# Optimization experiments

Hardware: AMD Instinct MI355X
Metric: run time of the kernel (lower is better)

## Reference

```python
import jax, jax.numpy as jnp
import numpy as np

LN_EPS = 1e-5


def setup_inputs() -> dict:
    key = jax.random.key(0)
    ks = jax.random.split(key, 8)
    B, N, E = 4, 512, 64
    s = 1.0 / np.sqrt(E)
    node_emb = jax.random.normal(ks[0], (B, N, E), dtype=jnp.float32)
    node_mask = jnp.ones((B, N), dtype=jnp.bool_)  # unused by forward, kept for fidelity
    ln_g = jnp.ones((E,), dtype=jnp.float32)
    ln_b = jnp.zeros((E,), dtype=jnp.float32)
    W1 = jax.random.normal(ks[1], (E, E), dtype=jnp.float32) * s
    b1 = jnp.zeros((E,), dtype=jnp.float32)
    W2 = jax.random.normal(ks[2], (E, E), dtype=jnp.float32) * s
    b2 = jnp.zeros((E,), dtype=jnp.float32)
    Wc = jax.random.normal(ks[3], (E, E * E), dtype=jnp.float32) / np.sqrt(E * E)
    bc = jnp.zeros((E,), dtype=jnp.float32)
    return {"node_emb": node_emb, "node_mask": node_mask, "ln_g": ln_g, "ln_b": ln_b,
            "W1": W1, "b1": b1, "W2": W2, "b2": b2, "Wc": Wc, "bc": bc}


def reference(node_emb, node_mask, ln_g, ln_b, W1, b1, W2, b2, Wc, bc):
    # node_emb: [B, N, E]; node_mask is unused (matches original module).
    E = node_emb.shape[-1]
    # LayerNorm over last dim (biased variance, like torch)
    mu = jnp.mean(node_emb, axis=-1, keepdims=True)
    var = jnp.mean(jnp.square(node_emb - mu), axis=-1, keepdims=True)
    h = (node_emb - mu) * jax.lax.rsqrt(var + LN_EPS) * ln_g + ln_b
    # Gated projections
    x = h * (jnp.einsum('bnd,od->bno', h, W1) + b1)   # left activations  [B,N,E]
    y = h * (jnp.einsum('bnd,od->bno', h, W2) + b2)   # right activations [B,N,E]
    # Original: matmul of [B,N*E,1] @ [B,1,N*E] then reshape/permute; analytically
    # R[b,i,d1,d2,j] = x[b,i,d1] * y[b,j,d2], flattened (d1,d2) fed to lin_cat.
    y2 = jnp.swapaxes(y, 1, 2)                        # [B, E, N]
    Wr = Wc.reshape(E, E, E)                          # Wr[o, d1, d2] = Wc[o, d1*E+d2]
    # Fused lin_cat: out[b,i,j,o] = sum_{d1,d2} x[b,i,d1] * y2[b,d2,j] * Wr[o,d1,d2] + bc[o]
    tmp = jnp.einsum('bid,ode->bioe', x, Wr)          # [B, N, E, E] (small)
    out = jnp.einsum('bioe,bej->bijo', tmp, y2) + bc  # [B, N, N, E]
    return out
```

## Files before the change

### kernel.cpp

```cpp
#include <hip/hip_runtime.h>
#include <hip/hip_bf16.h>


typedef __bf16 bf16x8 __attribute__((ext_vector_type(8)));
typedef unsigned short u16x8 __attribute__((ext_vector_type(8)));
typedef float f32x16 __attribute__((ext_vector_type(16)));

static __device__ inline unsigned short f2bf(float f) {
    unsigned int u = __float_as_uint(f);
    u = (u + 0x7FFFu + ((u >> 16) & 1u)) >> 16;
    return (unsigned short)u;
}

static __device__ inline bf16x8 load_frag(const unsigned short* p) {
    u16x8 t = *(const u16x8*)p;
    return __builtin_bit_cast(bf16x8, t);
}

__global__ __launch_bounds__(256) void ln_gate_kernel(
    const float* __restrict__ emb, const float* __restrict__ g,
    const float* __restrict__ bln,
    const float* __restrict__ W1, const float* __restrict__ b1,
    const float* __restrict__ W2, const float* __restrict__ b2,
    unsigned short* __restrict__ xo, unsigned short* __restrict__ yo)
{
    __shared__ float hsh[4][64];
    const int wave = threadIdx.x >> 6;
    const int lane = threadIdx.x & 63;
    const int row  = blockIdx.x * 4 + wave;

    float e = emb[row * 64 + lane];
    float s = e;
    #pragma unroll
    for (int m = 1; m < 64; m <<= 1) s += __shfl_xor(s, m);
    const float mu = s * (1.0f / 64.0f);
    const float d  = e - mu;
    float v = d * d;
    #pragma unroll
    for (int m = 1; m < 64; m <<= 1) v += __shfl_xor(v, m);
    const float rs = rsqrtf(v * (1.0f / 64.0f) + 1e-5f);
    const float h  = d * rs * g[lane] + bln[lane];

    hsh[wave][lane] = h;
    __syncthreads();

    const float4* hv  = (const float4*)hsh[wave];
    const float4* w1v = (const float4*)(W1 + lane * 64);
    const float4* w2v = (const float4*)(W2 + lane * 64);
    float d1 = 0.f, d2 = 0.f;
    #pragma unroll
    for (int k = 0; k < 16; k++) {
        float4 hh = hv[k];
        float4 a  = w1v[k];
        float4 c  = w2v[k];
        d1 += hh.x * a.x + hh.y * a.y + hh.z * a.z + hh.w * a.w;
        d2 += hh.x * c.x + hh.y * c.y + hh.z * c.z + hh.w * c.w;
    }
    xo[row * 64 + lane] = f2bf(h * (d1 + b1[lane]));
    yo[row * 64 + lane] = f2bf(h * (d2 + b2[lane]));
}

__global__ __launch_bounds__(256) void wcprep_kernel(
    const float* __restrict__ Wc, unsigned short* __restrict__ wt)
{
    __shared__ float t[64][65];
    const int o = blockIdx.x;
    const float* src = Wc + o * 4096;
    for (int w = threadIdx.x; w < 4096; w += 256)
        t[w >> 6][w & 63] = src[w];
    __syncthreads();
    unsigned short* dst = wt + o * 4096;
    for (int w = threadIdx.x; w < 4096; w += 256) {
        int d2 = w >> 6, d1 = w & 63;
        dst[w] = f2bf(t[d1][d2]);
    }
}

__global__ __launch_bounds__(256) void ugemm_kernel(
    const unsigned short* __restrict__ x, const unsigned short* __restrict__ wt,
    unsigned short* __restrict__ u)
{
    const int wave = threadIdx.x >> 6;
    const int lane = threadIdx.x & 63;
    const int m0 = blockIdx.x * 128 + (wave >> 1) * 64;
    const int n0 = blockIdx.y * 128 + (wave & 1) * 64;
    const int lr = lane & 31, lh = lane >> 5;

    bf16x8 af[2][4], bf[2][4];
    #pragma unroll
    for (int ks = 0; ks < 4; ks++) {
        const int k = ks * 16 + lh * 8;
        af[0][ks] = load_frag(x  + (m0      + lr) * 64 + k);
        af[1][ks] = load_frag(x  + (m0 + 32 + lr) * 64 + k);
        bf[0][ks] = load_frag(wt + (n0      + lr) * 64 + k);
        bf[1][ks] = load_frag(wt + (n0 + 32 + lr) * 64 + k);
    }
    f32x16 acc[2][2] = {};
    #pragma unroll
    for (int ks = 0; ks < 4; ks++) {
        acc[0][0] = __builtin_amdgcn_mfma_f32_32x32x16_bf16(af[0][ks], bf[0][ks], acc[0][0], 0, 0, 0);
        acc[0][1] = __builtin_amdgcn_mfma_f32_32x32x16_bf16(af[0][ks], bf[1][ks], acc[0][1], 0, 0, 0);
        acc[1][0] = __builtin_amdgcn_mfma_f32_32x32x16_bf16(af[1][ks], bf[0][ks], acc[1][0], 0, 0, 0);
        acc[1][1] = __builtin_amdgcn_mfma_f32_32x32x16_bf16(af[1][ks], bf[1][ks], acc[1][1], 0, 0, 0);
    }
    #pragma unroll
    for (int mi = 0; mi < 2; mi++)
        #pragma unroll
        for (int ni = 0; ni < 2; ni++)
            #pragma unroll
            for (int r = 0; r < 16; r++) {
                int row = m0 + mi * 32 + (r & 3) + 8 * (r >> 2) + 4 * lh;
                int col = n0 + ni * 32 + lr;
                u[row * 4096 + col] = f2bf(acc[mi][ni][r]);
            }
}

__global__ __launch_bounds__(256) void out_kernel(
    const unsigned short* __restrict__ y, const unsigned short* __restrict__ u,
    const float* __restrict__ bc, float* __restrict__ out)
{
    const int wave = threadIdx.x >> 6;
    const int lane = threadIdx.x & 63;
    const int mp = blockIdx.x;
    const int b  = mp >> 9;
    const int j0 = blockIdx.y * 256 + wave * 64;
    const int lr = lane & 31, lh = lane >> 5;

    const unsigned short* yb = y + b * (512 * 64);
    const unsigned short* ub = u + mp * 4096;

    bf16x8 af[2][4], bf[2][4];
    #pragma unroll
    for (int ks = 0; ks < 4; ks++) {
        const int k = ks * 16 + lh * 8;
        af[0][ks] = load_frag(yb + (j0      + lr) * 64 + k);
        af[1][ks] = load_frag(yb + (j0 + 32 + lr) * 64 + k);
        bf[0][ks] = load_frag(ub + (lr)      * 64 + k);
        bf[1][ks] = load_frag(ub + (32 + lr) * 64 + k);
    }
    f32x16 acc[2][2] = {};
    #pragma unroll
    for (int ks = 0; ks < 4; ks++) {
        acc[0][0] = __builtin_amdgcn_mfma_f32_32x32x16_bf16(af[0][ks], bf[0][ks], acc[0][0], 0, 0, 0);
        acc[0][1] = __builtin_amdgcn_mfma_f32_32x32x16_bf16(af[0][ks], bf[1][ks], acc[0][1], 0, 0, 0);
        acc[1][0] = __builtin_amdgcn_mfma_f32_32x32x16_bf16(af[1][ks], bf[0][ks], acc[1][0], 0, 0, 0);
        acc[1][1] = __builtin_amdgcn_mfma_f32_32x32x16_bf16(af[1][ks], bf[1][ks], acc[1][1], 0, 0, 0);
    }

    const float bias0 = bc[lr];
    const float bias1 = bc[32 + lr];
    float* outp = out + (size_t)mp * 32768;
    #pragma unroll
    for (int mi = 0; mi < 2; mi++)
        #pragma unroll
        for (int ni = 0; ni < 2; ni++) {
            const float bias = ni ? bias1 : bias0;
            const int col = ni * 32 + lr;
            #pragma unroll
            for (int r = 0; r < 16; r++) {
                int j = j0 + mi * 32 + (r & 3) + 8 * (r >> 2) + 4 * lh;
                __builtin_nontemporal_store(acc[mi][ni][r] + bias, &outp[j * 64 + col]);
            }
        }
}

extern "C" void kernel_launch(void* const* d_in, const int* in_sizes, int n_in,
                              void* d_out, int out_size, void* d_ws, size_t ws_size,
                              hipStream_t stream) {
    const float* emb  = (const float*)d_in[0];
    const float* ln_g = (const float*)d_in[2];
    const float* ln_b = (const float*)d_in[3];
    const float* W1   = (const float*)d_in[4];
    const float* b1   = (const float*)d_in[5];
    const float* W2   = (const float*)d_in[6];
    const float* b2   = (const float*)d_in[7];
    const float* Wc   = (const float*)d_in[8];
    const float* bc   = (const float*)d_in[9];
    float* out = (float*)d_out;

    char* ws = (char*)d_ws;
    unsigned short* x_ws  = (unsigned short*)(ws);
    unsigned short* y_ws  = (unsigned short*)(ws + 262144);
    unsigned short* wt_ws = (unsigned short*)(ws + 524288);
    unsigned short* u_ws  = (unsigned short*)(ws + 1048576);

    hipLaunchKernelGGL(ln_gate_kernel, dim3(512), dim3(256), 0, stream,
                       emb, ln_g, ln_b, W1, b1, W2, b2, x_ws, y_ws);
    hipLaunchKernelGGL(wcprep_kernel, dim3(64), dim3(256), 0, stream, Wc, wt_ws);
    hipLaunchKernelGGL(ugemm_kernel, dim3(16, 32), dim3(256), 0, stream,
                       x_ws, wt_ws, u_ws);
    hipLaunchKernelGGL(out_kernel, dim3(2048, 2), dim3(256), 0, stream,
                       y_ws, u_ws, bc, out);
}
```

Before: 315.9 us.

## Fuse u-GEMM into output kernel via LDS and merge prep kernels

Measured after the change: 323.9 us. +2.5%, slower.

```diff
diff --git a/kernel.cpp b/kernel.cpp
--- a/kernel.cpp
+++ b/kernel.cpp
@@ -1,10 +1,10 @@
 #include <hip/hip_runtime.h>
-#include <hip/hip_bf16.h>
 
 
 typedef __bf16 bf16x8 __attribute__((ext_vector_type(8)));
 typedef unsigned short u16x8 __attribute__((ext_vector_type(8)));
 typedef float f32x16 __attribute__((ext_vector_type(16)));
+typedef float f32x4  __attribute__((ext_vector_type(4)));
 
 static __device__ inline unsigned short f2bf(float f) {
     unsigned int u = __float_as_uint(f);
@@ -17,151 +17,150 @@
     return __builtin_bit_cast(bf16x8, t);
 }
 
-__global__ __launch_bounds__(256) void ln_gate_kernel(
+__global__ __launch_bounds__(256) void prep_kernel(
     const float* __restrict__ emb, const float* __restrict__ g,
     const float* __restrict__ bln,
     const float* __restrict__ W1, const float* __restrict__ b1,
     const float* __restrict__ W2, const float* __restrict__ b2,
-    unsigned short* __restrict__ xo, unsigned short* __restrict__ yo)
+    const float* __restrict__ Wc,
+    unsigned short* __restrict__ xo, unsigned short* __restrict__ yo,
+    unsigned short* __restrict__ wt)
 {
-    __shared__ float hsh[4][64];
-    const int wave = threadIdx.x >> 6;
-    const int lane = threadIdx.x & 63;
-    const int row  = blockIdx.x * 4 + wave;
+    __shared__ __align__(16) float smem[64 * 65];
+    const int bid = blockIdx.x;
 
-    float e = emb[row * 64 + lane];
-    float s = e;
-    #pragma unroll
-    for (int m = 1; m < 64; m <<= 1) s += __shfl_xor(s, m);
-    const float mu = s * (1.0f / 64.0f);
-    const float d  = e - mu;
-    float v = d * d;
-    #pragma unroll
-    for (int m = 1; m < 64; m <<= 1) v += __shfl_xor(v, m);
-    const float rs = rsqrtf(v * (1.0f / 64.0f) + 1e-5f);
-    const float h  = d * rs * g[lane] + bln[lane];
+    if (bid < 512) {
+        const int wave = threadIdx.x >> 6;
+        const int lane = threadIdx.x & 63;
+        const int row  = bid * 4 + wave;
 
-    hsh[wave][lane] = h;
-    __syncthreads();
+        float e = emb[row * 64 + lane];
+        float s = e;
+        #pragma unroll
+        for (int m = 1; m < 64; m <<= 1) s += __shfl_xor(s, m);
+        const float mu = s * (1.0f / 64.0f);
+        const float d  = e - mu;
+        float v = d * d;
+        #pragma unroll
+        for (int m = 1; m < 64; m <<= 1) v += __shfl_xor(v, m);
+        const float rs = rsqrtf(v * (1.0f / 64.0f) + 1e-5f);
+        const float h  = d * rs * g[lane] + bln[lane];
 
-    const float4* hv  = (const float4*)hsh[wave];
-    const float4* w1v = (const float4*)(W1 + lane * 64);
-    const float4* w2v = (const float4*)(W2 + lane * 64);
-    float d1 = 0.f, d2 = 0.f;
-    #pragma unroll
-    for (int k = 0; k < 16; k++) {
-        float4 hh = hv[k];
-        float4 a  = w1v[k];
-        float4 c  = w2v[k];
-        d1 += hh.x * a.x + hh.y * a.y + hh.z * a.z + hh.w * a.w;
-        d2 += hh.x * c.x + hh.y * c.y + hh.z * c.z + hh.w * c.w;
-    }
-    xo[row * 64 + lane] = f2bf(h * (d1 + b1[lane]));
-    yo[row * 64 + lane] = f2bf(h * (d2 + b2[lane]));
-}
+        float* hsh = smem + wave * 64;
+        hsh[lane] = h;
+        __syncthreads();
 
-__global__ __launch_bounds__(256) void wcprep_kernel(
-    const float* __restrict__ Wc, unsigned short* __restrict__ wt)
-{
-    __shared__ float t[64][65];
-    const int o = blockIdx.x;
-    const float* src = Wc + o * 4096;
-    for (int w = threadIdx.x; w < 4096; w += 256)
-        t[w >> 6][w & 63] = src[w];
-    __syncthreads();
-    unsigned short* dst = wt + o * 4096;
-    for (int w = threadIdx.x; w < 4096; w += 256) {
-        int d2 = w >> 6, d1 = w & 63;
-        dst[w] = f2bf(t[d1][d2]);
+        const float4* hv  = (const float4*)hsh;
+        const float4* w1v = (const float4*)(W1 + lane * 64);
+        const float4* w2v = (const float4*)(W2 + lane * 64);
+        float d1 = 0.f, d2 = 0.f;
+        #pragma unroll
+        for (int k = 0; k < 16; k++) {
+            float4 hh = hv[k];
+            float4 a  = w1v[k];
+            float4 c  = w2v[k];
+            d1 += hh.x * a.x + hh.y * a.y + hh.z * a.z + hh.w * a.w;
+            d2 += hh.x * c.x + hh.y * c.y + hh.z * c.z + hh.w * c.w;
+        }
+        xo[row * 64 + lane] = f2bf(h * (d1 + b1[lane]));
+        yo[row * 64 + lane] = f2bf(h * (d2 + b2[lane]));
+    } else {
+        float (*t)[65] = (float (*)[65])smem;
+        const int o = bid - 512;
+        const float* src = Wc + o * 4096;
+        for (int w = threadIdx.x; w < 4096; w += 256)
+            t[w >> 6][w & 63] = src[w];
+        __syncthreads();
+        unsigned short* dst = wt + o * 4096;
+        for (int w = threadIdx.x; w < 4096; w += 256) {
+            int d2 = w >> 6, d1 = w & 63;
+            dst[w] = f2bf(t[d1][d2]);
+        }
     }
 }
 
-__global__ __launch_bounds__(256) void ugemm_kernel(
-    const unsigned short* __restrict__ x, const unsigned short* __restrict__ wt,
-    unsigned short* __restrict__ u)
+__global__ __launch_bounds__(256) void uo_kernel(
+    const unsigned short* __restrict__ x, const unsigned short* __restrict__ y,
+    const unsigned short* __restrict__ wt, const float* __restrict__ bc,
+    float* __restrict__ out)
 {
+    __shared__ __align__(16) unsigned short su[4 * 4096];
+    __shared__ __align__(16) float st[4][32 * 64];
+
     const int wave = threadIdx.x >> 6;
     const int lane = threadIdx.x & 63;
-    const int m0 = blockIdx.x * 128 + (wave >> 1) * 64;
-    const int n0 = blockIdx.y * 128 + (wave & 1) * 64;
     const int lr = lane & 31, lh = lane >> 5;
+    const int mp0 = blockIdx.x * 4;
+    const int b   = mp0 >> 9;
 
-    bf16x8 af[2][4], bf[2][4];
+    const u16x8 zz = {};
+    bf16x8 xa[4];
     #pragma unroll
     for (int ks = 0; ks < 4; ks++) {
-        const int k = ks * 16 + lh * 8;
-        af[0][ks] = load_frag(x  + (m0      + lr) * 64 + k);
-        af[1][ks] = load_frag(x  + (m0 + 32 + lr) * 64 + k);
-        bf[0][ks] = load_frag(wt + (n0      + lr) * 64 + k);
-        bf[1][ks] = load_frag(wt + (n0 + 32 + lr) * 64 + k);
+        xa[ks] = (lr < 4)
+            ? load_frag(x + (mp0 + lr) * 64 + ks * 16 + lh * 8)
+            : __builtin_bit_cast(bf16x8, zz);
     }
-    f32x16 acc[2][2] = {};
-    #pragma unroll
-    for (int ks = 0; ks < 4; ks++) {
-        acc[0][0] = __builtin_amdgcn_mfma_f32_32x32x16_bf16(af[0][ks], bf[0][ks], acc[0][0], 0, 0, 0);
-        acc[0][1] = __builtin_amdgcn_mfma_f32_32x32x16_bf16(af[0][ks], bf[1][ks], acc[0][1], 0, 0, 0);
-        acc[1][0] = __builtin_amdgcn_mfma_f32_32x32x16_bf16(af[1][ks], bf[0][ks], acc[1][0], 0, 0, 0);
-        acc[1][1] = __builtin_amdgcn_mfma_f32_32x32x16_bf16(af[1][ks], bf[1][ks], acc[1][1], 0, 0, 0);
+
+    for (int i = 0; i < 32; i++) {
+        const int n0 = (wave * 32 + i) * 32;
+        bf16x8 bfr[4];
+        #pragma unroll
+        for (int ks = 0; ks < 4; ks++)
+            bfr[ks] = load_frag(wt + (n0 + lr) * 64 + ks * 16 + lh * 8);
+        f32x16 acc = {};
+        #pragma unroll
+        for (int ks = 0; ks < 4; ks++)
+            acc = __builtin_amdgcn_mfma_f32_32x32x16_bf16(xa[ks], bfr[ks], acc, 0, 0, 0);
+        if (lh == 0) {
+            const int o  = n0 >> 6;
+            const int d2 = (n0 & 63) + lr;
+            const int sw = (o & 7) << 3;
+            #pragma unroll
+            for (int r = 0; r < 4; r++)
+                su[(r * 4096 + o * 64 + d2) ^ sw] = f2bf(acc[r]);
+        }
     }
-    #pragma unroll
-    for (int mi = 0; mi < 2; mi++)
-        #pragma unroll
-        for (int ni = 0; ni < 2; ni++)
-            #pragma unroll
-            for (int r = 0; r < 16; r++) {
-                int row = m0 + mi * 32 + (r & 3) + 8 * (r >> 2) + 4 * lh;
-                int col = n0 + ni * 32 + lr;
-                u[row * 4096 + col] = f2bf(acc[mi][ni][r]);
-            }
-}
-
-__global__ __launch_bounds__(256) void out_kernel(
-    const unsigned short* __restrict__ y, const unsigned short* __restrict__ u,
-    const float* __restrict__ bc, float* __restrict__ out)
-{
-    const int wave = threadIdx.x >> 6;
-    const int lane = threadIdx.x & 63;
-    const int mp = blockIdx.x;
-    const int b  = mp >> 9;
-    const int j0 = blockIdx.y * 256 + wave * 64;
-    const int lr = lane & 31, lh = lane >> 5;
-
-    const unsigned short* yb = y + b * (512 * 64);
-    const unsigned short* ub = u + mp * 4096;
-
-    bf16x8 af[2][4], bf[2][4];
-    #pragma unroll
-    for (int ks = 0; ks < 4; ks++) {
-        const int k = ks * 16 + lh * 8;
-        af[0][ks] = load_frag(yb + (j0      + lr) * 64 + k);
-        af[1][ks] = load_frag(yb + (j0 + 32 + lr) * 64 + k);
-        bf[0][ks] = load_frag(ub + (lr)      * 64 + k);
-        bf[1][ks] = load_frag(ub + (32 + lr) * 64 + k);
-    }
-    f32x16 acc[2][2] = {};
-    #pragma unroll
-    for (int ks = 0; ks < 4; ks++) {
-        acc[0][0] = __builtin_amdgcn_mfma_f32_32x32x16_bf16(af[0][ks], bf[0][ks], acc[0][0], 0, 0, 0);
-        acc[0][1] = __builtin_amdgcn_mfma_f32_32x32x16_bf16(af[0][ks], bf[1][ks], acc[0][1], 0, 0, 0);
-        acc[1][0] = __builtin_amdgcn_mfma_f32_32x32x16_bf16(af[1][ks], bf[0][ks], acc[1][0], 0, 0, 0);
-        acc[1][1] = __builtin_amdgcn_mfma_f32_32x32x16_bf16(af[1][ks], bf[1][ks], acc[1][1], 0, 0, 0);
-    }
+    __syncthreads();
 
     const float bias0 = bc[lr];
     const float bias1 = bc[32 + lr];
-    float* outp = out + (size_t)mp * 32768;
-    #pragma unroll
-    for (int mi = 0; mi < 2; mi++)
+    const unsigned short* yb = y + b * (512 * 64);
+    float* st_w = st[wave];
+    const int swz = (lr & 7) << 3;
+
+    for (int jt = 0; jt < 4; jt++) {
+        const int j0 = wave * 128 + jt * 32;
+        bf16x8 af[4];
         #pragma unroll
-        for (int ni = 0; ni < 2; ni++) {
-            const float bias = ni ? bias1 : bias0;
-            const int col = ni * 32 + lr;
+        for (int ks = 0; ks < 4; ks++)
+            af[ks] = load_frag(yb + (j0 + lr) * 64 + ks * 16 + lh * 8);
+
+        #pragma unroll
+        for (int mp = 0; mp < 4; mp++) {
+            f32x16 acc0 = {}, acc1 = {};
+            #pragma unroll
+            for (int ks = 0; ks < 4; ks++) {
+                const int kofs = ks * 16 + lh * 8;
+                bf16x8 b0 = load_frag(&su[(mp * 4096 + lr * 64        + kofs) ^ swz]);
+                bf16x8 b1 = load_frag(&su[(mp * 4096 + (32 + lr) * 64 + kofs) ^ swz]);
+                acc0 = __builtin_amdgcn_mfma_f32_32x32x16_bf16(af[ks], b0, acc0, 0, 0, 0);
+                acc1 = __builtin_amdgcn_mfma_f32_32x32x16_bf16(af[ks], b1, acc1, 0, 0, 0);
+            }
             #pragma unroll
             for (int r = 0; r < 16; r++) {
-                int j = j0 + mi * 32 + (r & 3) + 8 * (r >> 2) + 4 * lh;
-                __builtin_nontemporal_store(acc[mi][ni][r] + bias, &outp[j * 64 + col]);
+                const int jl = (r & 3) + 8 * (r >> 2) + 4 * lh;
+                st_w[jl * 64 + lr]      = acc0[r] + bias0;
+                st_w[jl * 64 + 32 + lr] = acc1[r] + bias1;
+            }
+            float* outp = out + (size_t)(mp0 + mp) * 32768 + j0 * 64;
+            #pragma unroll
+            for (int q = 0; q < 8; q++) {
+                f32x4 v = *(const f32x4*)&st_w[q * 256 + lane * 4];
+                __builtin_nontemporal_store(v, (f32x4*)(outp + q * 256 + lane * 4));
             }
         }
+    }
 }
 
 extern "C" void kernel_launch(void* const* d_in, const int* in_sizes, int n_in,
@@ -182,13 +181,9 @@
     unsigned short* x_ws  = (unsigned short*)(ws);
     unsigned short* y_ws  = (unsigned short*)(ws + 262144);
     unsigned short* wt_ws = (unsigned short*)(ws + 524288);
-    unsigned short* u_ws  = (unsigned short*)(ws + 1048576);
 
-    hipLaunchKernelGGL(ln_gate_kernel, dim3(512), dim3(256), 0, stream,
-                       emb, ln_g, ln_b, W1, b1, W2, b2, x_ws, y_ws);
-    hipLaunchKernelGGL(wcprep_kernel, dim3(64), dim3(256), 0, stream, Wc, wt_ws);
-    hipLaunchKernelGGL(ugemm_kernel, dim3(16, 32), dim3(256), 0, stream,
-                       x_ws, wt_ws, u_ws);
-    hipLaunchKernelGGL(out_kernel, dim3(2048, 2), dim3(256), 0, stream,
-                       y_ws, u_ws, bc, out);
+    hipLaunchKernelGGL(prep_kernel, dim3(576), dim3(256), 0, stream,
+                       emb, ln_g, ln_b, W1, b1, W2, b2, Wc, x_ws, y_ws, wt_ws);
+    hipLaunchKernelGGL(uo_kernel, dim3(512), dim3(256), 0, stream,
+                       x_ws, y_ws, wt_ws, bc, out);
 }
```
